# Kernel optimization log

Measured on AMD Instinct MI355X. Metric: run time of the kernel, lower is better.

Reference implementation:

```python
import jax, jax.numpy as jnp
import numpy as np

N_NODES = 10000
N_EDGES = 128000


def _edge_conv(x, row, col, edge_attr, w1, b1, w2, b2):
    # gather endpoints, concat edge features, 2-layer MLP per edge
    m = jnp.concatenate([x[row], x[col], edge_attr], axis=1)  # [E, 2*in+edge]
    m = jax.nn.relu(m @ w1 + b1) @ w2 + b2                    # [E, out]
    # scatter-mean onto source nodes (flow='target_to_source' -> aggregate on row)
    n = x.shape[0]
    s = jax.ops.segment_sum(m, row, num_segments=n)
    cnt = jax.ops.segment_sum(jnp.ones((row.shape[0], 1), m.dtype), row, num_segments=n)
    out = s / jnp.maximum(cnt, 1.0)
    return out, m


def setup_inputs() -> dict:
    key = jax.random.key(0)
    ks = jax.random.split(key, 24)
    f = jnp.float32

    def lin(kw, kb, fan_in, fan_out):
        lim = 1.0 / np.sqrt(fan_in)
        w = jax.random.uniform(kw, (fan_in, fan_out), f, -lim, lim)
        b = jax.random.uniform(kb, (fan_out,), f, -lim, lim)
        return w, b

    inp = {}
    inp['x_org'] = jax.random.normal(ks[0], (N_NODES, 256), f)
    inp['x_rot'] = jax.random.normal(ks[1], (N_NODES, 4), f)
    inp['edge_index'] = jax.random.randint(ks[2], (2, N_EDGES), 0, N_NODES, jnp.int64 if jax.config.jax_enable_x64 else jnp.int32)
    inp['edge_attr'] = jax.random.normal(ks[3], (N_EDGES, 640), f)
    inp['edge_rot'] = jax.random.normal(ks[4], (N_EDGES, 4), f)

    # conv1: Linear(2*260+644=1164, 64), Linear(64, 64)
    inp['c1_w1'], inp['c1_b1'] = lin(ks[5], ks[6], 1164, 64)
    inp['c1_w2'], inp['c1_b2'] = lin(ks[7], ks[8], 64, 64)
    # conv2: Linear(2*64+704=832, 64), Linear(64, 64)
    inp['c2_w1'], inp['c2_b1'] = lin(ks[9], ks[10], 832, 64)
    inp['c2_w2'], inp['c2_b2'] = lin(ks[11], ks[12], 64, 64)
    # conv3: Linear(2*128+128=384, 64), Linear(64, 64)
    inp['c3_w1'], inp['c3_b1'] = lin(ks[13], ks[14], 384, 64)
    inp['c3_w2'], inp['c3_b2'] = lin(ks[15], ks[16], 64, 64)
    # conv4: Linear(384, 64), Linear(64, 64)
    inp['c4_w1'], inp['c4_b1'] = lin(ks[17], ks[18], 384, 64)
    inp['c4_w2'], inp['c4_b2'] = lin(ks[19], ks[20], 64, 64)
    # lin1: Linear(64, 4)
    inp['lin1_w'], inp['lin1_b'] = lin(ks[21], ks[22], 64, 4)
    # edge_fc: Linear(64, 32) -> ReLU -> Linear(32, 1)
    k23 = jax.random.split(ks[23], 4)
    inp['efc_w1'], inp['efc_b1'] = lin(k23[0], k23[1], 64, 32)
    inp['efc_w2'], inp['efc_b2'] = lin(k23[2], k23[3], 32, 1)
    return inp


def reference(x_org, x_rot, edge_index, edge_attr, edge_rot,
              c1_w1, c1_b1, c1_w2, c1_b2,
              c2_w1, c2_b1, c2_w2, c2_b2,
              c3_w1, c3_b1, c3_w2, c3_b2,
              c4_w1, c4_b1, c4_w2, c4_b2,
              lin1_w, lin1_b, efc_w1, efc_b1, efc_w2, efc_b2):
    node_feat = jnp.concatenate([x_org, x_rot], axis=1)
    edge_feat = jnp.concatenate([edge_attr, edge_rot], axis=1)
    row, col = edge_index[0], edge_index[1]
    E = edge_index.shape[1]

    x1, edge_x1 = _edge_conv(node_feat, row, col, edge_feat, c1_w1, c1_b1, c1_w2, c1_b2)
    edge_x1 = jax.nn.relu(edge_x1)

    x2, edge_x2 = _edge_conv(x1, row, col, jnp.concatenate([edge_attr, edge_x1], axis=1),
                             c2_w1, c2_b1, c2_w2, c2_b2)
    x2 = jax.nn.relu(x2)
    edge_x2 = jax.nn.relu(edge_x2)

    x3, edge_x3 = _edge_conv(jnp.concatenate([x2, x1], axis=1), row, col,
                             jnp.concatenate([edge_x2, edge_x1], axis=1),
                             c3_w1, c3_b1, c3_w2, c3_b2)
    x3 = jax.nn.relu(x3)
    edge_x3 = jax.nn.relu(edge_x3)

    x4, edge_x4 = _edge_conv(jnp.concatenate([x3, x2], axis=1), row, col,
                             jnp.concatenate([edge_x3, edge_x2], axis=1),
                             c4_w1, c4_b1, c4_w2, c4_b2)
    x4 = jax.nn.relu(x4)

    x = x4 @ lin1_w + lin1_b  # [N, 4]
    h = edge_x4[: E // 2] + edge_x4[E // 2:]
    pred_edge_res = jax.nn.relu(h @ efc_w1 + efc_b1) @ efc_w2 + efc_b2  # [E/2, 1]

    # F.normalize(x, p=2, dim=1)
    x = x / jnp.maximum(jnp.linalg.norm(x, axis=1, keepdims=True), 1e-12)
    return x, pred_edge_res
```

## Files before the change

kernel.cpp:

```cpp
#include <hip/hip_runtime.h>
#include <stdint.h>


#define N_NODES 10000
#define N_EDGES 128000
#define E_HALF  64000
#define NBLK    1000

typedef unsigned short u16;

using bf16x8 = __attribute__((ext_vector_type(8))) short;
using f32x4  = __attribute__((ext_vector_type(4))) float;

#define MFMA16(A, B, C) C = __builtin_amdgcn_mfma_f32_16x16x32_bf16(A, B, C, 0, 0, 0)

__device__ __align__(256) float g_acc[N_NODES * 64];
__device__ __align__(256) float g_deg[N_NODES];
__device__ __align__(256) float g_P[N_NODES * 128];
__device__ __align__(256) float g_x1[N_NODES * 64];
__device__ __align__(256) float g_x2[N_NODES * 64];
__device__ __align__(256) float g_x3[N_NODES * 64];
__device__ __align__(256) u16  g_fragA[(size_t)NBLK * 16384];
__device__ __align__(256) u16  g_fragB[(size_t)NBLK * 16384];
__device__ __align__(256) float g_Q2 [(size_t)NBLK * 8192];
__device__ __align__(256) float g_ex4[(size_t)N_EDGES * 64];
__device__ __align__(256) u16  g_wpA_hi[5 * 4096];
__device__ __align__(256) u16  g_wpA_lo[5 * 4096];
__device__ __align__(256) u16  g_wp2_hi[4 * 4096];
__device__ __align__(256) u16  g_wp2_lo[4 * 4096];
__device__ __align__(256) u16  g_wnp_hi[9 * 8192];
__device__ __align__(256) u16  g_wnp_lo[9 * 8192];
__device__ __align__(256) u16  g_wpC_hi[10 * 8192];
__device__ __align__(256) u16  g_wpC_lo[10 * 8192];
__device__ __align__(256) int g_row[N_EDGES];
__device__ __align__(256) int g_col[N_EDGES];
__device__ int g_mode;
__device__ int g_is64;

__device__ __forceinline__ float b2f(u16 u) {
    return __uint_as_float(((unsigned int)u) << 16);
}
__device__ __forceinline__ u16 f2b(float f) {
    unsigned int u = __float_as_uint(f);
    u += 0x7FFFu + ((u >> 16) & 1u);
    return (u16)(u >> 16);
}
__device__ __forceinline__ float ldf(const u16* p)   { return b2f(*p); }
__device__ __forceinline__ float ldf(const float* p) { return *p; }
__device__ __forceinline__ void  stf(u16* p, float v)   { *p = f2b(v); }
__device__ __forceinline__ void  stf(float* p, float v) { *p = v; }

__device__ __forceinline__ float4 load4(const float* p) { return *(const float4*)p; }
__device__ __forceinline__ float4 load4(const u16* p) {
    ushort4 v = *(const ushort4*)p;
    return make_float4(b2f(v.x), b2f(v.y), b2f(v.z), b2f(v.w));
}

__device__ __forceinline__ void gl_lds16(const void* g, void* l) {
    __builtin_amdgcn_global_load_lds(
        (const __attribute__((address_space(1))) void*)g,
        (__attribute__((address_space(3))) void*)l, 16, 0, 0);
}

__device__ __forceinline__ void split_pack(float4 v, uint2& hi, uint2& lo) {
    unsigned int ux = __float_as_uint(v.x), uy = __float_as_uint(v.y);
    unsigned int uz = __float_as_uint(v.z), uw = __float_as_uint(v.w);
    unsigned int hx = ux & 0xFFFF0000u, hy = uy & 0xFFFF0000u;
    unsigned int hz = uz & 0xFFFF0000u, hw = uw & 0xFFFF0000u;
    hi.x = (hx >> 16) | hy;
    hi.y = (hz >> 16) | hw;
    u16 lx = f2b(v.x - __uint_as_float(hx));
    u16 ly = f2b(v.y - __uint_as_float(hy));
    u16 lz = f2b(v.z - __uint_as_float(hz));
    u16 lw = f2b(v.w - __uint_as_float(hw));
    lo.x = (unsigned int)lx | ((unsigned int)ly << 16);
    lo.y = (unsigned int)lz | ((unsigned int)lw << 16);
}

__device__ __forceinline__ void mk_frag(float4 v0, float4 v1,
                                        bf16x8& fh, bf16x8& fl) {
    uint2 h0, l0, h1, l1;
    split_pack(v0, h0, l0);
    split_pack(v1, h1, l1);
    union { unsigned int w[4]; bf16x8 v; } H, L;
    H.w[0] = h0.x; H.w[1] = h0.y; H.w[2] = h1.x; H.w[3] = h1.y;
    L.w[0] = l0.x; L.w[1] = l0.y; L.w[2] = l1.x; L.w[3] = l1.y;
    fh = H.v; fl = L.v;
}

__global__ void prologue_a(const void* x_org_v, const int* __restrict__ eidx) {
    const int i = blockIdx.x * 256 + threadIdx.x;
    g_acc[i] = 0.f;
    if (i < N_NODES) g_deg[i] = 0.f;
    if (blockIdx.x == 0 && threadIdx.x < 64) {
        const u16* w = (const u16*)x_org_v;
        const int t = threadIdx.x;
        int ok = 0;
        for (int j = t; j < 128; j += 64) {
            u16 v = w[j];
            int ex = (v >> 7) & 0xFF;
            ok += ((ex >= 0x68 && ex <= 0x88) || ((v & 0x7FFFu) == 0)) ? 1 : 0;
        }
        #pragma unroll
        for (int off = 32; off >= 1; off >>= 1) ok += __shfl_xor(ok, off);
        bool allz = true;
        for (int j = t; j < 2048; j += 64) allz = allz && (eidx[2 * j + 1] == 0);
        unsigned long long m = __ballot(allz);
        if (t == 0) {
            g_mode = (ok >= 110) ? 0 : 1;
            g_is64 = (m == ~0ull) ? 1 : 0;
        }
    }
}

__device__ __forceinline__ void pack_pair(u16* dh, u16* dl, float v) {
    const u16 hh = f2b(v);
    *dh = hh; *dl = f2b(v - b2f(hh));
}
template<typename TW>
__device__ void pack_wnp(const TW* w, int hioff, int rem, u16* dh, u16* dl) {
    const int s = rem >> 13, kt = (rem >> 12) & 1, ct = (rem >> 9) & 7,
              l = (rem >> 3) & 63, r = rem & 7;
    const int k = s * 64 + kt * 32 + 4 * (l >> 4) + (r & 3) + 16 * (r >> 2);
    const int col = ct * 16 + (l & 15);
    const int row = (col < 64) ? k : (hioff + k);
    pack_pair(dh + rem, dl + rem, ldf(w + (size_t)row * 64 + (col & 63)));
}
template<typename TW>
__device__ void pack_wpa(const TW* w, int we, int rem, u16* dh, u16* dl) {
    const int s = rem >> 12, kt = (rem >> 11) & 1, ct = (rem >> 9) & 3,
              l = (rem >> 3) & 63, r = rem & 7;
    const int k = s * 64 + kt * 32 + 4 * (l >> 4) + (r & 3) + 16 * (r >> 2);
    pack_pair(dh + rem, dl + rem,
              ldf(w + (size_t)(we + k) * 64 + ct * 16 + (l & 15)));
}
template<typename TW>
__device__ void pack_wpc(const TW* w1, const TW* w2w, int rem) {
    const int s = rem >> 13, kt = (rem >> 12) & 1, ct = (rem >> 9) & 7,
              l = (rem >> 3) & 63, r = rem & 7;
    const int k = s * 64 + kt * 32 + 4 * (l >> 4) + (r & 3) + 16 * (r >> 2);
    const int col = ct * 16 + (l & 15);
    float v = (col < 64) ? ldf(w1 + (size_t)(520 + k) * 64 + col)
                         : ldf(w2w + (size_t)(128 + k) * 64 + (col - 64));
    pack_pair(g_wpC_hi + rem, g_wpC_lo + rem, v);
}

template<typename TW>
__device__ void pack_all_body(const TW* c1w1, const TW* c1w2, const TW* c2w1,
        const TW* c2w2, const TW* c3w1, const TW* c3w2, const TW* c4w1,
        const TW* c4w2) {
    const int idx = blockIdx.x * 256 + threadIdx.x;
    if (idx < 81920)        pack_wpc<TW>(c1w1, c2w1, idx);
    else if (idx < 114688)  pack_wnp<TW>(c1w1, 260, idx - 81920,  g_wnp_hi,            g_wnp_lo);
    else if (idx < 122880)  pack_wnp<TW>(c2w1, 64,  idx - 114688, g_wnp_hi + 4 * 8192, g_wnp_lo + 4 * 8192);
    else if (idx < 139264)  pack_wnp<TW>(c3w1, 128, idx - 122880, g_wnp_hi + 5 * 8192, g_wnp_lo + 5 * 8192);
    else if (idx < 155648)  pack_wnp<TW>(c4w1, 128, idx - 139264, g_wnp_hi + 7 * 8192, g_wnp_lo + 7 * 8192);
    else if (idx < 159744)  pack_wpa<TW>(c2w1, 768, idx - 155648, g_wpA_hi,            g_wpA_lo);
    else if (idx < 167936)  pack_wpa<TW>(c3w1, 256, idx - 159744, g_wpA_hi + 4096,     g_wpA_lo + 4096);
    else if (idx < 176128)  pack_wpa<TW>(c4w1, 256, idx - 167936, g_wpA_hi + 12288,    g_wpA_lo + 12288);
    else if (idx < 180224)  pack_wpa<TW>(c1w2, 0,   idx - 176128, g_wp2_hi,            g_wp2_lo);
    else if (idx < 184320)  pack_wpa<TW>(c2w2, 0,   idx - 180224, g_wp2_hi + 4096,     g_wp2_lo + 4096);
    else if (idx < 188416)  pack_wpa<TW>(c3w2, 0,   idx - 184320, g_wp2_hi + 8192,     g_wp2_lo + 8192);
    else if (idx < 192512)  pack_wpa<TW>(c4w2, 0,   idx - 188416, g_wp2_hi + 12288,    g_wp2_lo + 12288);
}

__global__ void prep_k(const void* c1w1, const void* c1w2, const void* c2w1,
        const void* c2w2, const void* c3w1, const void* c3w2, const void* c4w1,
        const void* c4w2, const int* __restrict__ eidx) {
    if ((int)blockIdx.x < 752) {
        if (g_mode == 0)
            pack_all_body<u16>((const u16*)c1w1, (const u16*)c1w2, (const u16*)c2w1,
                (const u16*)c2w2, (const u16*)c3w1, (const u16*)c3w2,
                (const u16*)c4w1, (const u16*)c4w2);
        else
            pack_all_body<float>((const float*)c1w1, (const float*)c1w2,
                (const float*)c2w1, (const float*)c2w2, (const float*)c3w1,
                (const float*)c3w2, (const float*)c4w1, (const float*)c4w2);
    } else {
        const int e = ((int)blockIdx.x - 752) * 256 + threadIdx.x;
        int row, col;
        if (g_is64) { row = eidx[2 * e]; col = eidx[2 * (e + N_EDGES)]; }
        else        { row = eidx[e];     col = eidx[e + N_EDGES]; }
        g_row[e] = row; g_col[e] = col;
        atomicAdd(&g_deg[row], 1.0f);
    }
}

template<typename TA>
__device__ void node_mfma_in_body(float* smrot, float* smwt,
        const TA* A1, const TA* rotsrc, const TA* w1, float* P) {
    const int t = threadIdx.x;
    const int lane = t & 63, wid = t >> 6;
    const int q = lane >> 4, n = lane & 15;
    const int r0b = blockIdx.x * 64;

    if (t < 64) {
        const int rr = min(r0b + t, N_NODES - 1);
        float4 v = load4(rotsrc + (size_t)rr * 4);
        smrot[t * 4 + 0] = v.x; smrot[t * 4 + 1] = v.y;
        smrot[t * 4 + 2] = v.z; smrot[t * 4 + 3] = v.w;
    }
    for (int i = t; i < 512; i += 256) {
        const int j = i >> 7, c = i & 127;
        const int row = (c < 64) ? (256 + j) : (516 + j);
        smwt[i] = ldf(w1 + (size_t)row * 64 + (c & 63));
    }
    __syncthreads();

    const int arow = min(r0b + wid * 16 + n, N_NODES - 1);

    f32x4 acc[8];
    #pragma unroll
    for (int ct = 0; ct < 8; ++ct) acc[ct] = (f32x4){0.f, 0.f, 0.f, 0.f};

    #pragma unroll
    for (int s = 0; s < 4; ++s) {
        #pragma unroll
        for (int kt = 0; kt < 2; ++kt) {
            const TA* p = A1 + (size_t)arow * 256 + s * 64 + kt * 32 + q * 4;
            float4 v0 = load4(p), v1 = load4(p + 16);
            bf16x8 ah, al;
            mk_frag(v0, v1, ah, al);
            const u16* wph = g_wnp_hi + s * 8192;
            const u16* wpl = g_wnp_lo + s * 8192;
            #pragma unroll
            for (int ct = 0; ct < 8; ++ct) {
                bf16x8 bh = *(const bf16x8*)&wph[(kt * 8 + ct) * 512 + lane * 8];
                bf16x8 bl = *(const bf16x8*)&wpl[(kt * 8 + ct) * 512 + lane * 8];
                MFMA16(ah, bh, acc[ct]);
                MFMA16(al, bh, acc[ct]);
                MFMA16(ah, bl, acc[ct]);
            }
        }
    }

    #pragma unroll
    for (int ct = 0; ct < 8; ++ct) {
        #pragma unroll
        for (int i = 0; i < 4; ++i) {
            const int rl = wid * 16 + 4 * q + i;
            const int row = r0b + rl;
            const int col = ct * 16 + n;
            float v = acc[ct][i]
                    + smrot[rl * 4 + 0] * smwt[0 * 128 + col]
                    + smrot[rl * 4 + 1] * smwt[1 * 128 + col]
                    + smrot[rl * 4 + 2] * smwt[2 * 128 + col]
                    + smrot[rl * 4 + 3] * smwt[3 * 128 + col];
            if (row < N_NODES) P[(size_t)row * 128 + col] = v;
        }
    }
}

__global__ void __launch_bounds__(256) node_mfma_in(
        const void* A1, const void* rotsrc, const void* w1, float* __restrict__ P) {
    __shared__ float smrot[256], smwt[512];
    if (g_mode == 0)
        node_mfma_in_body<u16>(smrot, smwt, (const u16*)A1, (const u16*)rotsrc,
                               (const u16*)w1, P);
    else
        node_mfma_in_body<float>(smrot, smwt, (const float*)A1, (const float*)rotsrc,
                               (const float*)w1, P);
}

template<int NS2, bool RELU>
__global__ void __launch_bounds__(256) node_mfma_acc(
        const float* A2, float* __restrict__ xout, float* __restrict__ P,
        int wnpoff) {
    const int t = threadIdx.x;
    const int lane = t & 63, wid = t >> 6;
    const int q = lane >> 4, n = lane & 15;
    const int r0b = blockIdx.x * 64;
    const int rown = r0b + wid * 16 + n;
    const int arow = min(rown, N_NODES - 1);
    const bool own = rown < N_NODES;
    const float inv = 1.0f / fmaxf(g_deg[arow], 1.0f);

    f32x4 acc[8];
    #pragma unroll
    for (int ct = 0; ct < 8; ++ct) acc[ct] = (f32x4){0.f, 0.f, 0.f, 0.f};

    #pragma unroll
    for (int kt = 0; kt < 2; ++kt) {
        float* p = g_acc + (size_t)arow * 64 + kt * 32 + q * 4;
        float4 v0 = load4(p), v1 = load4(p + 16);
        v0.x *= inv; v0.y *= inv; v0.z *= inv; v0.w *= inv;
        v1.x *= inv; v1.y *= inv; v1.z *= inv; v1.w *= inv;
        if (RELU) {
            v0.x = fmaxf(v0.x, 0.f); v0.y = fmaxf(v0.y, 0.f);
            v0.z = fmaxf(v0.z, 0.f); v0.w = fmaxf(v0.w, 0.f);
            v1.x = fmaxf(v1.x, 0.f); v1.y = fmaxf(v1.y, 0.f);
            v1.z = fmaxf(v1.z, 0.f); v1.w = fmaxf(v1.w, 0.f);
        }
        if (own) {
            *(float4*)(xout + (size_t)arow * 64 + kt * 32 + q * 4) = v0;
            *(float4*)(xout + (size_t)arow * 64 + kt * 32 + q * 4 + 16) = v1;
            *(float4*)p = make_float4(0.f, 0.f, 0.f, 0.f);
            *(float4*)(p + 16) = make_float4(0.f, 0.f, 0.f, 0.f);
        }
        bf16x8 ah, al;
        mk_frag(v0, v1, ah, al);
        const u16* wph = g_wnp_hi + wnpoff;
        const u16* wpl = g_wnp_lo + wnpoff;
        #pragma unroll
        for (int ct = 0; ct < 8; ++ct) {
            bf16x8 bh = *(const bf16x8*)&wph[(kt * 8 + ct) * 512 + lane * 8];
            bf16x8 bl = *(const bf16x8*)&wpl[(kt * 8 + ct) * 512 + lane * 8];
            MFMA16(ah, bh, acc[ct]);
            MFMA16(al, bh, acc[ct]);
            MFMA16(ah, bl, acc[ct]);
        }
    }
    if constexpr (NS2 > 0) {
        #pragma unroll
        for (int kt = 0; kt < 2; ++kt) {
            const float* p = A2 + (size_t)arow * 64 + kt * 32 + q * 4;
            float4 v0 = load4(p), v1 = load4(p + 16);
            bf16x8 ah, al;
            mk_frag(v0, v1, ah, al);
            const u16* wph = g_wnp_hi + wnpoff + 8192;
            const u16* wpl = g_wnp_lo + wnpoff + 8192;
            #pragma unroll
            for (int ct = 0; ct < 8; ++ct) {
                bf16x8 bh = *(const bf16x8*)&wph[(kt * 8 + ct) * 512 + lane * 8];
                bf16x8 bl = *(const bf16x8*)&wpl[(kt * 8 + ct) * 512 + lane * 8];
                MFMA16(ah, bh, acc[ct]);
                MFMA16(al, bh, acc[ct]);
                MFMA16(ah, bl, acc[ct]);
            }
        }
    }

    #pragma unroll
    for (int ct = 0; ct < 8; ++ct) {
        #pragma unroll
        for (int i = 0; i < 4; ++i) {
            const int rl = wid * 16 + 4 * q + i;
            const int row = r0b + rl;
            if (row < N_NODES) P[(size_t)row * 128 + ct * 16 + n] = acc[ct][i];
        }
    }
}

__device__ __forceinline__ void frag_store_o(u16* hreg, int wid, int lane,
        const f32x4 (&oacc)[2][4], u16* Fdst, int blkid) {
    const int q = lane >> 4, n = lane & 15;
    #pragma unroll
    for (int rt = 0; rt < 2; ++rt)
        #pragma unroll
        for (int ct = 0; ct < 4; ++ct)
            #pragma unroll
            for (int i = 0; i < 4; ++i) {
                float v = fmaxf(oacc[rt][ct][i], 0.f);
                unsigned int hb = __float_as_uint(v) & 0xFFFF0000u;
                const u16 hh = (u16)(hb >> 16);
                const u16 hl = f2b(v - __uint_as_float(hb));
                const int off = wid * 4096
                              + (((ct >> 1) * 2 + rt) * 64 + (n >> 2) * 16 + 4 * q + i) * 8
                              + (ct & 1) * 4 + (n & 3);
                hreg[off]        = hh;
                hreg[off + 2048] = hl;
            }
    #pragma unroll
    for (int kt = 0; kt < 2; ++kt)
        #pragma unroll
        for (int rtl = 0; rtl < 2; ++rtl) {
            const int src = wid * 4096 + ((kt * 2 + rtl) * 64 + lane) * 8;
            bf16x8 h8 = *(const bf16x8*)&hreg[src];
            bf16x8 l8 = *(const bf16x8*)&hreg[src + 2048];
            const size_t gb = (size_t)blkid * 16384
                            + (size_t)(kt * 8 + wid * 2 + rtl) * 512 + lane * 8;
            *(bf16x8*)&Fdst[gb]        = h8;
            *(bf16x8*)&Fdst[gb + 8192] = l8;
        }
}

template<typename TA, typename TW>
__device__ void edge_c1_body(u16* smW, int* srow, int* scol,
        float* b1s, float* b2s, float* rot, float* wtl,
        const TA* efa, const TA* rotsrc,
        const TW* w1, const TW* b1v, const TW* b2v) {
    const int t = threadIdx.x;
    const int lane = t & 63, wid = t >> 6;
    const int q = lane >> 4, n = lane & 15;
    const int e0 = blockIdx.x * 128;

    #pragma unroll
    for (int i = 0; i < 4; ++i) {
        const int L = wid * 4096 + i * 1024;
        const char* src = (L < 8192) ? (const char*)g_wp2_hi + L
                                     : (const char*)g_wp2_lo + (L - 8192);
        gl_lds16(src + lane * 16, (char*)smW + 32768 + L);
    }

    if (t < 128) srow[t] = g_row[e0 + t];
    else         scol[t - 128] = g_col[e0 + t - 128];
    if (t >= 128 && t < 192) b1s[t - 128] = ldf(b1v + (t - 128));
    if (t >= 192)            b2s[t - 192] = ldf(b2v + (t - 192));
    if (t < 128) {
        float4 r4 = load4(rotsrc + (size_t)(e0 + t) * 4);
        rot[t * 4 + 0] = r4.x; rot[t * 4 + 1] = r4.y;
        rot[t * 4 + 2] = r4.z; rot[t * 4 + 3] = r4.w;
    }
    wtl[t] = ldf(w1 + (size_t)(1160 + (t >> 6)) * 64 + (t & 63));

    const TA* arow0 = efa + (size_t)(e0 + wid * 32 + n) * 640;
    const TA* arow1 = efa + (size_t)(e0 + wid * 32 + 16 + n) * 640;

    f32x4 acc[2][8];
    #pragma unroll
    for (int a_ = 0; a_ < 2; ++a_)
        #pragma unroll
        for (int b_ = 0; b_ < 8; ++b_)
            acc[a_][b_] = (f32x4){0.f, 0.f, 0.f, 0.f};

    auto stageW = [&](int h) {
        const char* sh = (const char*)g_wpC_hi + (size_t)h * 8192;
        const char* sl = (const char*)g_wpC_lo + (size_t)h * 8192;
        char* d = (char*)smW + (h & 1) * 16384;
        #pragma unroll
        for (int i = 0; i < 2; ++i) {
            const int off = wid * 2048 + i * 1024;
            gl_lds16(sh + off + lane * 16, d + off);
            gl_lds16(sl + off + lane * 16, d + 8192 + off);
        }
    };

    float4 abuf[3][2][2];
    auto issueA = [&](float4 (&buf)[2][2], int h) {
        const int cb = (h >> 1) * 64 + (h & 1) * 32 + q * 4;
        buf[0][0] = load4(arow0 + cb);
        buf[0][1] = load4(arow0 + cb + 16);
        buf[1][0] = load4(arow1 + cb);
        buf[1][1] = load4(arow1 + cb + 16);
    };
    auto step = [&](float4 (&buf)[2][2], int h) {
        const int wb = (h & 1) * 8192;
        bf16x8 ah0, al0, ah1, al1;
        mk_frag(buf[0][0], buf[0][1], ah0, al0);
        mk_frag(buf[1][0], buf[1][1], ah1, al1);
        #pragma unroll
        for (int ct = 0; ct < 8; ++ct) {
            bf16x8 bh = *(const bf16x8*)&smW[wb + ct * 512 + lane * 8];
            bf16x8 bl = *(const bf16x8*)&smW[wb + 4096 + ct * 512 + lane * 8];
            MFMA16(ah0, bh, acc[0][ct]);
            MFMA16(ah1, bh, acc[1][ct]);
            MFMA16(al0, bh, acc[0][ct]);
            MFMA16(al1, bh, acc[1][ct]);
            MFMA16(ah0, bl, acc[0][ct]);
            MFMA16(ah1, bl, acc[1][ct]);
        }
    };

    stageW(0);
    issueA(abuf[0], 0);
    issueA(abuf[1], 1);
    __builtin_amdgcn_sched_barrier(0);
    asm volatile("s_waitcnt vmcnt(8) lgkmcnt(0)");
    __builtin_amdgcn_sched_barrier(0);
    __builtin_amdgcn_s_barrier();

    #pragma unroll
    for (int h = 0; h < 20; ++h) {
        if (h < 19) stageW(h + 1);
        __builtin_amdgcn_sched_barrier(0);
        if (h == 19) asm volatile("s_waitcnt vmcnt(0)");
        else         asm volatile("s_waitcnt vmcnt(8)");
        __builtin_amdgcn_sched_barrier(0);
        __builtin_amdgcn_s_barrier();
        if (h < 18) issueA(abuf[(h + 2) % 3], h + 2);
        step(abuf[h % 3], h);
        __builtin_amdgcn_s_barrier();
    }

    {
        float* qf = g_Q2 + (size_t)blockIdx.x * 8192 + (size_t)t * 32;
        #pragma unroll
        for (int rt = 0; rt < 2; ++rt)
            #pragma unroll
            for (int c2 = 0; c2 < 4; ++c2)
                *(f32x4*)(qf + rt * 16 + c2 * 4) = acc[rt][4 + c2];
    }

    u16* hreg = smW;
    #pragma unroll
    for (int rt = 0; rt < 2; ++rt)
        #pragma unroll
        for (int ct = 0; ct < 4; ++ct)
            #pragma unroll
            for (int i = 0; i < 4; ++i) {
                const int rl = wid * 32 + rt * 16 + 4 * q + i;
                const int col = ct * 16 + n;
                float v = acc[rt][ct][i] + b1s[col]
                        + g_P[(size_t)srow[rl] * 128 + col]
                        + g_P[(size_t)scol[rl] * 128 + 64 + col]
                        + rot[rl * 4 + 0] * wtl[0 * 64 + col]
                        + rot[rl * 4 + 1] * wtl[1 * 64 + col]
                        + rot[rl * 4 + 2] * wtl[2 * 64 + col]
                        + rot[rl * 4 + 3] * wtl[3 * 64 + col];
                v = fmaxf(v, 0.f);
                unsigned int hb = __float_as_uint(v) & 0xFFFF0000u;
                const u16 hh = (u16)(hb >> 16);
                const u16 hl = f2b(v - __uint_as_float(hb));
                const int off = wid * 4096
                              + (((ct >> 1) * 2 + rt) * 64 + (n >> 2) * 16 + 4 * q + i) * 8
                              + (ct & 1) * 4 + (n & 3);
                hreg[off]        = hh;
                hreg[off + 2048] = hl;
            }

    f32x4 oacc[2][4];
    #pragma unroll
    for (int rt = 0; rt < 2; ++rt)
        #pragma unroll
        for (int ct = 0; ct < 4; ++ct) {
            const float bb = b2s[ct * 16 + n];
            oacc[rt][ct] = (f32x4){bb, bb, bb, bb};
        }
    #pragma unroll
    for (int kt = 0; kt < 2; ++kt) {
        const int r0 = wid * 4096 + ((kt * 2 + 0) * 64 + lane) * 8;
        const int r1 = wid * 4096 + ((kt * 2 + 1) * 64 + lane) * 8;
        bf16x8 ah0 = *(const bf16x8*)&hreg[r0];
        bf16x8 ah1 = *(const bf16x8*)&hreg[r1];
        bf16x8 al0 = *(const bf16x8*)&hreg[r0 + 2048];
        bf16x8 al1 = *(const bf16x8*)&hreg[r1 + 2048];
        #pragma unroll
        for (int ct = 0; ct < 4; ++ct) {
            bf16x8 bh = *(const bf16x8*)&smW[16384 + (kt * 4 + ct) * 512 + lane * 8];
            bf16x8 bl = *(const bf16x8*)&smW[20480 + (kt * 4 + ct) * 512 + lane * 8];
            MFMA16(ah0, bh, oacc[0][ct]);
            MFMA16(ah1, bh, oacc[1][ct]);
            MFMA16(al0, bh, oacc[0][ct]);
            MFMA16(al1, bh, oacc[1][ct]);
            MFMA16(ah0, bl, oacc[0][ct]);
            MFMA16(ah1, bl, oacc[1][ct]);
        }
    }

    #pragma unroll
    for (int rt = 0; rt < 2; ++rt)
        #pragma unroll
        for (int ct = 0; ct < 4; ++ct)
            #pragma unroll
            for (int i = 0; i < 4; ++i) {
                const int rl = wid * 32 + rt * 16 + 4 * q + i;
                atomicAdd(&g_acc[(size_t)srow[rl] * 64 + ct * 16 + n], oacc[rt][ct][i]);
            }
    frag_store_o(hreg, wid, lane, oacc, g_fragA, blockIdx.x);
}

__global__ void __launch_bounds__(256, 3) edge_c1(
        const void* efa, const void* rotsrc,
        const void* w1, const void* b1, const void* b2) {
    __shared__ __align__(16) u16 smW[24576];
    __shared__ int srow[128], scol[128];
    __shared__ float b1s[64], b2s[64], rot[512], wtl[256];
    if (g_mode == 0)
        edge_c1_body<u16, u16>(smW, srow, scol, b1s, b2s, rot, wtl,
            (const u16*)efa, (const u16*)rotsrc,
            (const u16*)w1, (const u16*)b1, (const u16*)b2);
    else
        edge_c1_body<float, float>(smW, srow, scol, b1s, b2s, rot, wtl,
            (const float*)efa, (const float*)rotsrc,
            (const float*)w1, (const float*)b1, (const float*)b2);
}

template<typename TW, int NSF, bool HASQ2, bool FRAG_OUT>
__device__ void edge_lite_body(u16* smW, int* srow, int* scol,
        float* b1s, float* b2s,
        const u16* f0, const u16* f1,
        const TW* b1v, const TW* b2v, u16* Ffrag, float* fout,
        int wpAoff, int wp2off) {
    const int t = threadIdx.x;
    const int lane = t & 63, wid = t >> 6;
    const int q = lane >> 4, n = lane & 15;
    const int e0 = blockIdx.x * 128;
    const size_t blkb = (size_t)blockIdx.x * 16384;
    constexpr int N2 = 16384;

    #pragma unroll
    for (int i = 0; i < (NSF + 1) * 4; ++i) {
        const int j = i * 4 + wid;
        const char* src;
        int dstB;
        if (j < NSF * 8) {
            src = (const char*)(g_wpA_hi + wpAoff) + j * 1024;            dstB = j * 1024;
        } else if (j < NSF * 16) {
            src = (const char*)(g_wpA_lo + wpAoff) + (j - NSF * 8) * 1024; dstB = j * 1024;
        } else if (j < NSF * 16 + 8) {
            src = (const char*)(g_wp2_hi + wp2off) + (j - NSF * 16) * 1024;
            dstB = 32768 + (j - NSF * 16) * 1024;
        } else {
            src = (const char*)(g_wp2_lo + wp2off) + (j - NSF * 16 - 8) * 1024;
            dstB = 32768 + (j - NSF * 16) * 1024;
        }
        gl_lds16(src + lane * 16, (char*)smW + dstB);
    }

    if (t < 128) srow[t] = g_row[e0 + t];
    else         scol[t - 128] = g_col[e0 + t - 128];
    if (t >= 128 && t < 192) b1s[t - 128] = ldf(b1v + (t - 128));
    if (t >= 192)            b2s[t - 192] = ldf(b2v + (t - 192));
    __syncthreads();

    float pr[2][4][4], pc[2][4][4];
    #pragma unroll
    for (int rt = 0; rt < 2; ++rt)
        #pragma unroll
        for (int ct = 0; ct < 4; ++ct)
            #pragma unroll
            for (int i = 0; i < 4; ++i) {
                const int rl = wid * 32 + rt * 16 + 4 * q + i;
                const int col = ct * 16 + n;
                pr[rt][ct][i] = g_P[(size_t)srow[rl] * 128 + col];
                pc[rt][ct][i] = g_P[(size_t)scol[rl] * 128 + 64 + col];
            }

    f32x4 acc[2][4];
    #pragma unroll
    for (int a_ = 0; a_ < 2; ++a_)
        #pragma unroll
        for (int b_ = 0; b_ < 4; ++b_)
            acc[a_][b_] = (f32x4){0.f, 0.f, 0.f, 0.f};

    #pragma unroll
    for (int s = 0; s < NSF; ++s) {
        const u16* fs = (s == 0) ? f0 : f1;
        #pragma unroll
        for (int kt = 0; kt < 2; ++kt) {
            const size_t ba0 = blkb + (size_t)(kt * 8 + wid * 2 + 0) * 512 + lane * 8;
            const size_t ba1 = blkb + (size_t)(kt * 8 + wid * 2 + 1) * 512 + lane * 8;
            bf16x8 ah0 = *(const bf16x8*)&fs[ba0];
            bf16x8 al0 = *(const bf16x8*)&fs[ba0 + 8192];
            bf16x8 ah1 = *(const bf16x8*)&fs[ba1];
            bf16x8 al1 = *(const bf16x8*)&fs[ba1 + 8192];
            #pragma unroll
            for (int ct = 0; ct < 4; ++ct) {
                bf16x8 bh = *(const bf16x8*)&smW[s * 4096 + (kt * 4 + ct) * 512 + lane * 8];
                bf16x8 bl = *(const bf16x8*)&smW[NSF * 4096 + s * 4096 + (kt * 4 + ct) * 512 + lane * 8];
                MFMA16(ah0, bh, acc[0][ct]);
                MFMA16(ah1, bh, acc[1][ct]);
                MFMA16(al0, bh, acc[0][ct]);
                MFMA16(al1, bh, acc[1][ct]);
                MFMA16(ah0, bl, acc[0][ct]);
                MFMA16(ah1, bl, acc[1][ct]);
            }
        }
    }

    __builtin_amdgcn_s_barrier();
    u16* hreg = smW;

    const float* qf = g_Q2 + (size_t)blockIdx.x * 8192 + (size_t)t * 32;
    #pragma unroll
    for (int rt = 0; rt < 2; ++rt)
        #pragma unroll
        for (int ct = 0; ct < 4; ++ct) {
            f32x4 qv;
            if constexpr (HASQ2) qv = *(const f32x4*)(qf + rt * 16 + ct * 4);
            #pragma unroll
            for (int i = 0; i < 4; ++i) {
                const int rl = wid * 32 + rt * 16 + 4 * q + i;
                const int col = ct * 16 + n;
                float v = acc[rt][ct][i] + b1s[col]
                        + pr[rt][ct][i] + pc[rt][ct][i];
                if constexpr (HASQ2) v += qv[i];
                v = fmaxf(v, 0.f);
                unsigned int hb = __float_as_uint(v) & 0xFFFF0000u;
                const u16 hh = (u16)(hb >> 16);
                const u16 hl = f2b(v - __uint_as_float(hb));
                const int off = wid * 4096
                              + (((ct >> 1) * 2 + rt) * 64 + (n >> 2) * 16 + 4 * q + i) * 8
                              + (ct & 1) * 4 + (n & 3);
                hreg[off]        = hh;
                hreg[off + 2048] = hl;
            }
        }

    f32x4 oacc[2][4];
    #pragma unroll
    for (int rt = 0; rt < 2; ++rt)
        #pragma unroll
        for (int ct = 0; ct < 4; ++ct) {
            const float bb = b2s[ct * 16 + n];
            oacc[rt][ct] = (f32x4){bb, bb, bb, bb};
        }
    #pragma unroll
    for (int kt = 0; kt < 2; ++kt) {
        const int r0 = wid * 4096 + ((kt * 2 + 0) * 64 + lane) * 8;
        const int r1 = wid * 4096 + ((kt * 2 + 1) * 64 + lane) * 8;
        bf16x8 ah0 = *(const bf16x8*)&hreg[r0];
        bf16x8 ah1 = *(const bf16x8*)&hreg[r1];
        bf16x8 al0 = *(const bf16x8*)&hreg[r0 + 2048];
        bf16x8 al1 = *(const bf16x8*)&hreg[r1 + 2048];
        #pragma unroll
        for (int ct = 0; ct < 4; ++ct) {
            bf16x8 bh = *(const bf16x8*)&smW[N2 + (kt * 4 + ct) * 512 + lane * 8];
            bf16x8 bl = *(const bf16x8*)&smW[N2 + 4096 + (kt * 4 + ct) * 512 + lane * 8];
            MFMA16(ah0, bh, oacc[0][ct]);
            MFMA16(ah1, bh, oacc[1][ct]);
            MFMA16(al0, bh, oacc[0][ct]);
            MFMA16(al1, bh, oacc[1][ct]);
            MFMA16(ah0, bl, oacc[0][ct]);
            MFMA16(ah1, bl, oacc[1][ct]);
        }
    }

    #pragma unroll
    for (int rt = 0; rt < 2; ++rt)
        #pragma unroll
        for (int ct = 0; ct < 4; ++ct)
            #pragma unroll
            for (int i = 0; i < 4; ++i) {
                const int rl = wid * 32 + rt * 16 + 4 * q + i;
                const int col = ct * 16 + n;
                const float v = oacc[rt][ct][i];
                atomicAdd(&g_acc[(size_t)srow[rl] * 64 + col], v);
                if constexpr (!FRAG_OUT)
                    fout[(size_t)(e0 + rl) * 64 + col] = v;
            }
    if constexpr (FRAG_OUT)
        frag_store_o(hreg, wid, lane, oacc, Ffrag, blockIdx.x);
}

template<int NSF, bool HASQ2, bool FRAG_OUT>
__global__ void __launch_bounds__(256, 3) edge_lite(
        const u16* f0, const u16* f1, const void* b1, const void* b2,
        u16* Ffrag, float* fout, int wpAoff, int wp2off) {
    __shared__ __align__(16) u16 smW[24576];
    __shared__ int srow[128], scol[128];
    __shared__ float b1s[64], b2s[64];
    if (g_mode == 0)
        edge_lite_body<u16, NSF, HASQ2, FRAG_OUT>(smW, srow, scol, b1s, b2s,
            f0, f1, (const u16*)b1, (const u16*)b2, Ffrag, fout, wpAoff, wp2off);
    else
        edge_lite_body<float, NSF, HASQ2, FRAG_OUT>(smW, srow, scol, b1s, b2s,
            f0, f1, (const float*)b1, (const float*)b2, Ffrag, fout, wpAoff, wp2off);
}

template<typename T>
__device__ void final_node_body(const T* w, const T* b, T* out, int bid) {
    const int t = threadIdx.x;
    const int lane = t & 63;
    const int n = bid * 4 + (t >> 6);
    float inv = 1.0f / fmaxf(g_deg[n], 1.0f);
    float x4 = fmaxf(g_acc[(size_t)n * 64 + lane] * inv, 0.0f);
    float r[4];
    #pragma unroll
    for (int j = 0; j < 4; ++j) {
        float v = x4 * ldf(w + lane * 4 + j);
        #pragma unroll
        for (int off = 32; off >= 1; off >>= 1) v += __shfl_xor(v, off);
        r[j] = v + ldf(b + j);
    }
    float nrm = sqrtf(r[0]*r[0] + r[1]*r[1] + r[2]*r[2] + r[3]*r[3]);
    float dn = fmaxf(nrm, 1e-12f);
    if (lane < 4) stf(out + n * 4 + lane, r[lane] / dn);
}

template<typename T>
__device__ void edge_head_body(const float* ex4, const T* w1, const T* b1,
                               const T* w2, const T* b2, T* out, int bid) {
    __shared__ float lw1[2048];
    __shared__ float lw2[32];
    const int t = threadIdx.x;
    for (int i = t; i < 2048; i += 256) lw1[i] = ldf(w1 + i);
    if (t < 32) lw2[t] = ldf(w2 + t);
    __syncthreads();
    const int e = bid * 256 + t;
    float a[32];
    #pragma unroll
    for (int j = 0; j < 32; ++j) a[j] = ldf(b1 + j);
    const float* p0 = ex4 + (size_t)e * 64;
    const float* p1 = ex4 + (size_t)(e + E_HALF) * 64;
    for (int c = 0; c < 64; ++c) {
        float h = p0[c] + p1[c];
        #pragma unroll
        for (int j = 0; j < 32; ++j) a[j] += h * lw1[c * 32 + j];
    }
    float s = ldf(b2);
    #pragma unroll
    for (int j = 0; j < 32; ++j) s += fmaxf(a[j], 0.f) * lw2[j];
    stf(out + e, s);
}

__global__ void __launch_bounds__(256) tail_k(
        const void* lw, const void* lb, const float* ex4,
        const void* ew1, const void* eb1, const void* ew2, const void* eb2,
        void* out) {
    const int b = blockIdx.x;
    if (b < 2500) {
        if (g_mode == 0) final_node_body<u16>((const u16*)lw, (const u16*)lb, (u16*)out, b);
        else             final_node_body<float>((const float*)lw, (const float*)lb, (float*)out, b);
    } else {
        if (g_mode == 0)
            edge_head_body<u16>(ex4, (const u16*)ew1, (const u16*)eb1,
                (const u16*)ew2, (const u16*)eb2, (u16*)out + 40000, b - 2500);
        else
            edge_head_body<float>(ex4, (const float*)ew1, (const float*)eb1,
                (const float*)ew2, (const float*)eb2, (float*)out + 40000, b - 2500);
    }
}

__global__ void sentinel_fill(unsigned int* out, int n_words) {
    int i = blockIdx.x * 256 + threadIdx.x;
    if (i < n_words) out[i] = 0x44794479u;
}

static void* sym_addr(const void* symbol) {
    void* p = nullptr;
    (void)hipGetSymbolAddress(&p, symbol);
    return p;
}

extern "C" void kernel_launch(void* const* d_in, const int* in_sizes, int n_in,
                              void* d_out, int out_size, void* d_ws, size_t ws_size,
                              hipStream_t stream) {
    (void)d_ws; (void)ws_size;
    bool ok = (n_in == 27) && (out_size == 104000)
           && (in_sizes[0] == 2560000) && (in_sizes[2] == 256000)
           && (in_sizes[3] == 81920000) && (in_sizes[5] == 74496)
           && (in_sizes[21] == 256) && (in_sizes[25] == 32);
    if (!ok) {
        sentinel_fill<<<204, 256, 0, stream>>>((unsigned int*)d_out, 52000);
        return;
    }
    const void* x_org     = d_in[0];
    const void* x_rot     = d_in[1];
    const int*  eidx      = (const int*)d_in[2];
    const void* edge_attr = d_in[3];
    const void* edge_rot  = d_in[4];

    float* P   = (float*)sym_addr(HIP_SYMBOL(g_P));
    float* x1  = (float*)sym_addr(HIP_SYMBOL(g_x1));
    float* x2  = (float*)sym_addr(HIP_SYMBOL(g_x2));
    float* x3  = (float*)sym_addr(HIP_SYMBOL(g_x3));
    u16*   fA  = (u16*)sym_addr(HIP_SYMBOL(g_fragA));
    u16*   fB  = (u16*)sym_addr(HIP_SYMBOL(g_fragB));
    float* ex4 = (float*)sym_addr(HIP_SYMBOL(g_ex4));

    prologue_a<<<2500, 256, 0, stream>>>(x_org, eidx);
    prep_k<<<1252, 256, 0, stream>>>(d_in[5], d_in[7], d_in[9], d_in[11],
                                     d_in[13], d_in[15], d_in[17], d_in[19], eidx);

    node_mfma_in<<<157, 256, 0, stream>>>(x_org, x_rot, d_in[5], P);
    edge_c1<<<NBLK, 256, 0, stream>>>(edge_attr, edge_rot, d_in[5], d_in[6], d_in[8]);

    node_mfma_acc<0, false><<<157, 256, 0, stream>>>(nullptr, x1, P, 4 * 8192);
    edge_lite<1, true, true><<<NBLK, 256, 0, stream>>>(
        fA, nullptr, d_in[10], d_in[12], fB, nullptr, 0, 4096);

    node_mfma_acc<1, true><<<157, 256, 0, stream>>>(x1, x2, P, 5 * 8192);
    edge_lite<2, false, true><<<NBLK, 256, 0, stream>>>(
        fB, fA, d_in[14], d_in[16], fA, nullptr, 4096, 8192);
    node_mfma_acc<1, true><<<157, 256, 0, stream>>>(x2, x3, P, 7 * 8192);
    edge_lite<2, false, false><<<NBLK, 256, 0, stream>>>(
        fA, fB, d_in[18], d_in[20], nullptr, ex4, 12288, 12288);

    tail_k<<<2750, 256, 0, stream>>>(d_in[21], d_in[22], ex4,
                                     d_in[23], d_in[24], d_in[25], d_in[26], d_out);
}
```

Baseline: 824.3 us.

## Triple-buffer weight staging in edge_c1 and drop per-step trailing barrier

The edge_c1 K-loop moves from double to triple buffering of the staged weight tiles in LDS and from three to four register buffers for the A rows. This lets each step issue the next weight stage and A prefetch before waiting, and removes the second barrier per iteration. It also raises wave priority around the MFMA step. LDS use grows to 64 KB, so launch bounds drop from 3 to 2 blocks per CU, trading occupancy for deeper prefetch.

```diff
diff --git a/kernel.cpp b/kernel.cpp
--- a/kernel.cpp
+++ b/kernel.cpp
@@ -389,7 +389,7 @@
         const int L = wid * 4096 + i * 1024;
         const char* src = (L < 8192) ? (const char*)g_wp2_hi + L
                                      : (const char*)g_wp2_lo + (L - 8192);
-        gl_lds16(src + lane * 16, (char*)smW + 32768 + L);
+        gl_lds16(src + lane * 16, (char*)smW + 49152 + L);
     }
 
     if (t < 128) srow[t] = g_row[e0 + t];
@@ -413,10 +413,10 @@
         for (int b_ = 0; b_ < 8; ++b_)
             acc[a_][b_] = (f32x4){0.f, 0.f, 0.f, 0.f};
 
-    auto stageW = [&](int h) {
+    auto stageW = [&](int h, int bufbyte) {
         const char* sh = (const char*)g_wpC_hi + (size_t)h * 8192;
         const char* sl = (const char*)g_wpC_lo + (size_t)h * 8192;
-        char* d = (char*)smW + (h & 1) * 16384;
+        char* d = (char*)smW + bufbyte;
         #pragma unroll
         for (int i = 0; i < 2; ++i) {
             const int off = wid * 2048 + i * 1024;
@@ -424,8 +424,6 @@
             gl_lds16(sl + off + lane * 16, d + 8192 + off);
         }
     };
-
-    float4 abuf[3][2][2];
     auto issueA = [&](float4 (&buf)[2][2], int h) {
         const int cb = (h >> 1) * 64 + (h & 1) * 32 + q * 4;
         buf[0][0] = load4(arow0 + cb);
@@ -433,15 +431,14 @@
         buf[1][0] = load4(arow1 + cb);
         buf[1][1] = load4(arow1 + cb + 16);
     };
-    auto step = [&](float4 (&buf)[2][2], int h) {
-        const int wb = (h & 1) * 8192;
+    auto step = [&](float4 (&buf)[2][2], int wb_u16) {
         bf16x8 ah0, al0, ah1, al1;
         mk_frag(buf[0][0], buf[0][1], ah0, al0);
         mk_frag(buf[1][0], buf[1][1], ah1, al1);
         #pragma unroll
         for (int ct = 0; ct < 8; ++ct) {
-            bf16x8 bh = *(const bf16x8*)&smW[wb + ct * 512 + lane * 8];
-            bf16x8 bl = *(const bf16x8*)&smW[wb + 4096 + ct * 512 + lane * 8];
+            bf16x8 bh = *(const bf16x8*)&smW[wb_u16 + ct * 512 + lane * 8];
+            bf16x8 bl = *(const bf16x8*)&smW[wb_u16 + 4096 + ct * 512 + lane * 8];
             MFMA16(ah0, bh, acc[0][ct]);
             MFMA16(ah1, bh, acc[1][ct]);
             MFMA16(al0, bh, acc[0][ct]);
@@ -451,26 +448,42 @@
         }
     };
 
-    stageW(0);
-    issueA(abuf[0], 0);
-    issueA(abuf[1], 1);
+    float4 a0[2][2], a1[2][2], a2[2][2], a3[2][2];
+
+    stageW(0, 0);
+    issueA(a0, 0);
+    issueA(a1, 1);
     __builtin_amdgcn_sched_barrier(0);
-    asm volatile("s_waitcnt vmcnt(8) lgkmcnt(0)");
+    asm volatile("s_waitcnt vmcnt(12) lgkmcnt(0)");
     __builtin_amdgcn_sched_barrier(0);
     __builtin_amdgcn_s_barrier();
 
-    #pragma unroll
-    for (int h = 0; h < 20; ++h) {
-        if (h < 19) stageW(h + 1);
-        __builtin_amdgcn_sched_barrier(0);
-        if (h == 19) asm volatile("s_waitcnt vmcnt(0)");
-        else         asm volatile("s_waitcnt vmcnt(8)");
-        __builtin_amdgcn_sched_barrier(0);
-        __builtin_amdgcn_s_barrier();
-        if (h < 18) issueA(abuf[(h + 2) % 3], h + 2);
-        step(abuf[h % 3], h);
-        __builtin_amdgcn_s_barrier();
-    }
+#define C1B(H, AC, AN, VM)                                                    \
+    do {                                                                      \
+        if constexpr ((H) < 19) stageW((H) + 1, (((H) + 1) % 3) * 16384);     \
+        if constexpr ((H) < 18) issueA(AN, (H) + 2);                          \
+        __builtin_amdgcn_sched_barrier(0);                                    \
+        asm volatile("s_waitcnt vmcnt(" VM ")");                              \
+        __builtin_amdgcn_sched_barrier(0);                                    \
+        __builtin_amdgcn_s_barrier();                                         \
+        __builtin_amdgcn_s_setprio(1);                                        \
+        step(AC, ((H) % 3) * 8192);                                           \
+        __builtin_amdgcn_s_setprio(0);                                        \
+    } while (0)
+
+    C1B(0,  a0, a2, "12"); C1B(1,  a1, a3, "12");
+    C1B(2,  a2, a0, "12"); C1B(3,  a3, a1, "12");
+    C1B(4,  a0, a2, "12"); C1B(5,  a1, a3, "12");
+    C1B(6,  a2, a0, "12"); C1B(7,  a3, a1, "12");
+    C1B(8,  a0, a2, "12"); C1B(9,  a1, a3, "12");
+    C1B(10, a2, a0, "12"); C1B(11, a3, a1, "12");
+    C1B(12, a0, a2, "12"); C1B(13, a1, a3, "12");
+    C1B(14, a2, a0, "12"); C1B(15, a3, a1, "12");
+    C1B(16, a0, a2, "12"); C1B(17, a1, a3, "12");
+    C1B(18, a2, a0, "8");  C1B(19, a3, a1, "0");
+#undef C1B
+
+    __builtin_amdgcn_s_barrier();
 
     {
         float* qf = g_Q2 + (size_t)blockIdx.x * 8192 + (size_t)t * 32;
@@ -526,8 +539,8 @@
         bf16x8 al1 = *(const bf16x8*)&hreg[r1 + 2048];
         #pragma unroll
         for (int ct = 0; ct < 4; ++ct) {
-            bf16x8 bh = *(const bf16x8*)&smW[16384 + (kt * 4 + ct) * 512 + lane * 8];
-            bf16x8 bl = *(const bf16x8*)&smW[20480 + (kt * 4 + ct) * 512 + lane * 8];
+            bf16x8 bh = *(const bf16x8*)&smW[24576 + (kt * 4 + ct) * 512 + lane * 8];
+            bf16x8 bl = *(const bf16x8*)&smW[28672 + (kt * 4 + ct) * 512 + lane * 8];
             MFMA16(ah0, bh, oacc[0][ct]);
             MFMA16(ah1, bh, oacc[1][ct]);
             MFMA16(al0, bh, oacc[0][ct]);
@@ -549,10 +562,10 @@
     frag_store_o(hreg, wid, lane, oacc, g_fragA, blockIdx.x);
 }
 
-__global__ void __launch_bounds__(256, 3) edge_c1(
+__global__ void __launch_bounds__(256, 2) edge_c1(
         const void* efa, const void* rotsrc,
         const void* w1, const void* b1, const void* b2) {
-    __shared__ __align__(16) u16 smW[24576];
+    __shared__ __align__(16) u16 smW[32768];
     __shared__ int srow[128], scol[128];
     __shared__ float b1s[64], b2s[64], rot[512], wtl[256];
     if (g_mode == 0)
```

Measured after the change: 801.1 us (median of 3 runs). 1.03x faster.
